# Kernel optimization log

Hardware: AMD Instinct MI355X
Metric: run time of the kernel (lower is better)

## Reference

```python
import jax, jax.numpy as jnp
import numpy as np

K = 3
TAPS = K * K
STD = float(np.sqrt(2.0)) / K  # FilterNorm scale: relu gain / kernel_size


def filter_norm(f, axis):
    # torch FilterNorm: subtract mean, divide by unbiased std (+1e-10), scale by STD
    m = jnp.mean(f, axis=axis, keepdims=True)
    sd = jnp.std(f, axis=axis, keepdims=True, ddof=1)
    return (f - m) / (sd + 1e-10) * STD


def setup_inputs() -> dict:
    key = jax.random.key(0)
    ks = jax.random.split(key, 9)
    B, C, H, W = 4, 64, 192, 192
    mid = int(C * 0.2)  # se_ratio=0.2 -> 12
    f = lambda k, shape, s: jax.random.normal(k, shape, jnp.float32) * s
    return {
        'x':   f(ks[0], (B, C, H, W), 1.0),
        'sw':  f(ks[1], (TAPS, C), 0.05),        # spatial branch 1x1 conv weight
        'sb':  f(ks[2], (TAPS,), 0.05),
        'cw1': f(ks[3], (mid, C), 0.05),         # channel branch squeeze
        'cb1': f(ks[4], (mid,), 0.05),
        'cw2': f(ks[5], (C * TAPS, mid), 0.05),  # channel branch expand
        'cb2': f(ks[6], (C * TAPS,), 0.05),
        'w2':  f(ks[7], (C, C, 1, 9), 0.05),     # trailing 1x9 conv
        'b2':  f(ks[8], (C,), 0.05),
    }


def block_forward(x, sw, sb, cw1, cb1, cw2, cb2, w2, b2):
    B, C, H, W = x.shape
    # --- DDFPack ---
    # spatial filters: 1x1 conv -> (B, 9, H, W), FilterNorm across the 9 taps
    s = jnp.einsum('bchw,tc->bthw', x, sw) + sb[None, :, None, None]
    s = filter_norm(s, axis=1)
    # channel filters: GAP -> 1x1 -> relu -> 1x1 -> (B, C, 9), FilterNorm over taps
    g = x.mean(axis=(2, 3))                         # (B, C)
    h1 = jax.nn.relu(g @ cw1.T + cb1)               # (B, mid)
    cf = (h1 @ cw2.T + cb2).reshape(B, C, TAPS)     # (B, C, 9)
    cf = filter_norm(cf, axis=2)
    # decoupled dynamic filter apply: per-pixel depthwise 3x3, combine='mul', pad=1
    xp = jnp.pad(x, ((0, 0), (0, 0), (1, 1), (1, 1)))
    out = jnp.zeros_like(x)
    for idx in range(TAPS):  # fixed 9-tap loop, no big unfold intermediate
        i, j = idx // K, idx % K
        out = out + xp[:, :, i:i + H, j:j + W] * s[:, idx:idx + 1] * cf[:, :, idx, None, None]
    # --- LeakyReLU(0.1) -> 1x9 conv (pad (0,4)) -> residual add (res_scale=1) ---
    a = jnp.where(out >= 0, out, 0.1 * out)
    y = jax.lax.conv_general_dilated(a, w2, (1, 1), ((0, 0), (4, 4)),
                                     dimension_numbers=('NCHW', 'OIHW', 'NCHW'))
    y = y + b2[None, :, None, None]
    return x + y


def reference(x, sw, sb, cw1, cb1, cw2, cb2, w2, b2):
    return block_forward(x, sw, sb, cw1, cb1, cw2, cb2, w2, b2)
```

## Files before the change

### kernel.cpp

```cpp
#include <hip/hip_runtime.h>
#include <hip/hip_bf16.h>

#define B_    4
#define C_    64
#define H_    192
#define W_    192
#define TAPS_ 9
#define MID_  12
#define HW_   (H_ * W_)
#define K_TOT 576
#define AT_STRIDE 72

constexpr float STD_ = 0.47140452079103173f;

using bf16 = __hip_bfloat16;
typedef __attribute__((ext_vector_type(4))) float  f32x4;
typedef __attribute__((ext_vector_type(8))) short  short8;

__device__ __forceinline__ unsigned short f2bf_bits(float v) {
    union { bf16 h; unsigned short u; } cv;
    cv.h = __float2bfloat16(v);
    return cv.u;
}

__device__ __forceinline__ int at_word(int row, int cw) {
    int key = (row >> 2) & 7;
    return row * (AT_STRIDE / 2) + ((((cw >> 2) ^ key) & 7) << 2) + (cw & 3);
}

__global__ __launch_bounds__(256) void k_pre(const float* __restrict__ x,
                                             const float* __restrict__ w2,
                                             unsigned short* __restrict__ w2bf,
                                             float* __restrict__ partials) {
    int bx = blockIdx.x;
    if (bx < 144) {
        int d = bx * 256 + threadIdx.x;
        int o = d / K_TOT;
        int rem = d - o * K_TOT;
        int t = rem >> 6;
        int c = rem & 63;
        w2bf[d] = f2bf_bits(w2[(o * C_ + c) * TAPS_ + t]);
        return;
    }
    bx -= 144;
    int bc = bx / 3, part = bx - 3 * (bx / 3);
    const float4* p = (const float4*)(x + (size_t)bc * HW_ + part * 12288);
    float s = 0.f;
    #pragma unroll
    for (int k = 0; k < 12; ++k) {
        float4 u = p[threadIdx.x + k * 256];
        s += u.x + u.y + u.z + u.w;
    }
    #pragma unroll
    for (int off = 32; off; off >>= 1) s += __shfl_down(s, off);
    __shared__ float red[4];
    if ((threadIdx.x & 63) == 0) red[threadIdx.x >> 6] = s;
    __syncthreads();
    if (threadIdx.x == 0)
        partials[bx] = red[0] + red[1] + red[2] + red[3];
}

__global__ __launch_bounds__(256) void k_cf(const float* __restrict__ partials,
                                            const float* __restrict__ cw1,
                                            const float* __restrict__ cb1,
                                            const float* __restrict__ cw2,
                                            const float* __restrict__ cb2,
                                            float* __restrict__ cfn) {
    __shared__ float g_l[B_ * C_];
    __shared__ float h1_l[B_ * MID_];
    int tid = threadIdx.x;
    g_l[tid] = (partials[tid * 3] + partials[tid * 3 + 1] + partials[tid * 3 + 2])
               * (1.0f / HW_);
    __syncthreads();
    if (tid < B_ * MID_) {
        int b = tid / MID_, m = tid % MID_;
        float acc = cb1[m];
        for (int c = 0; c < C_; ++c) acc += g_l[b * C_ + c] * cw1[m * C_ + c];
        h1_l[tid] = fmaxf(acc, 0.f);
    }
    __syncthreads();
    int b = tid >> 6, c = tid & 63;
    float f[TAPS_];
    float mean = 0.f;
    #pragma unroll
    for (int t = 0; t < TAPS_; ++t) {
        int n = c * TAPS_ + t;
        float acc = cb2[n];
        #pragma unroll
        for (int m = 0; m < MID_; ++m) acc += h1_l[b * MID_ + m] * cw2[n * MID_ + m];
        f[t] = acc;
        mean += acc;
    }
    mean *= (1.f / TAPS_);
    float var = 0.f;
    #pragma unroll
    for (int t = 0; t < TAPS_; ++t) { float d = f[t] - mean; var += d * d; }
    var *= (1.f / (TAPS_ - 1));
    float scale = STD_ / (sqrtf(fmaxf(var, 0.f)) + 1e-10f);
    #pragma unroll
    for (int t = 0; t < TAPS_; ++t)
        cfn[(b * C_ + c) * TAPS_ + t] = (f[t] - mean) * scale;
}

__global__ __launch_bounds__(256, 3) void k_main(const float* __restrict__ x,
                                                 const float* __restrict__ sw,
                                                 const float* __restrict__ sb,
                                                 const float* __restrict__ cfn,
                                                 const unsigned short* __restrict__ w2bf,
                                                 const float* __restrict__ bias2,
                                                 float* __restrict__ out) {
    __shared__ __align__(16) char smem[36016];
    short*          aT   = (short*)smem;
    unsigned*       aT32 = (unsigned*)smem;
    float*          sw_l = (float*)smem;
    float*          s_l  = (float*)(smem + 28800);
    float*          b2_l = (float*)(smem + 35712);
    float*          sb_l = (float*)(smem + 35968);

    int bh = blockIdx.x;
    int bb = bh / H_;
    int h  = bh - bb * H_;
    int tid = threadIdx.x;
    int lane = tid & 63, wid = tid >> 6;
    int quad = lane >> 4, l16 = lane & 15;
    int obase = wid * 16;

    for (int i = tid; i < TAPS_ * C_; i += 256) sw_l[i] = sw[i];
    if (tid < C_) b2_l[tid] = bias2[tid];
    if (tid < TAPS_) sb_l[tid] = sb[tid];
    __syncthreads();

    const short* w2s = (const short*)w2bf;
    const short* arow = w2s + (obase + l16) * K_TOT + quad * 8;
    short8 a0 = *(const short8*)(arow);
    short8 a1 = *(const short8*)(arow + 32);

    if (tid < W_) {
        int w = tid;
        float acc[TAPS_];
        #pragma unroll
        for (int t = 0; t < TAPS_; ++t) acc[t] = sb_l[t];
        const float* px = x + (size_t)bb * C_ * HW_ + h * W_ + w;
        #pragma unroll 8
        for (int c = 0; c < C_; ++c) {
            float xv = px[(size_t)c * HW_];
            #pragma unroll
            for (int t = 0; t < TAPS_; ++t) acc[t] = fmaf(xv, sw_l[t * C_ + c], acc[t]);
        }
        float mean = 0.f;
        #pragma unroll
        for (int t = 0; t < TAPS_; ++t) mean += acc[t];
        mean *= (1.f / TAPS_);
        float var = 0.f;
        #pragma unroll
        for (int t = 0; t < TAPS_; ++t) { float d = acc[t] - mean; var += d * d; }
        var *= (1.f / (TAPS_ - 1));
        float scale = STD_ / (sqrtf(fmaxf(var, 0.f)) + 1e-10f);
        float* sp = s_l + (w & 3) * 432 + (w >> 2);
        #pragma unroll
        for (int t = 0; t < TAPS_; ++t) sp[t * 48] = (acc[t] - mean) * scale;
    }
    __syncthreads();

    for (int i = tid; i < 8 * (AT_STRIDE / 2); i += 256) {
        int rowIdx = i / (AT_STRIDE / 2);
        int col    = i - rowIdx * (AT_STRIDE / 2);
        int r = (rowIdx < 4) ? rowIdx : (192 + rowIdx);
        aT32[r * (AT_STRIDE / 2) + col] = 0u;
    }

    {
        int wbase = wid * 16;
        if (lane < 48) {
            int w0 = 4 * lane;
            float sreg[4][TAPS_];
            #pragma unroll
            for (int k = 0; k < 4; ++k) {
                const float* sp = s_l + k * 432 + lane;
                #pragma unroll
                for (int t = 0; t < TAPS_; ++t) sreg[k][t] = sp[t * 48];
            }
            bool l0 = (lane == 0), l47 = (lane == 47);
            int rok0 = (h > 0), rok2 = (h < H_ - 1);
            int midx = l0 ? 0 : (w0 - 1);
            int pidx = l47 ? w0 : (w0 + 4);
            const float* xbase = x + (long)bb * C_ * HW_ + (long)(h - 1) * W_;
            #pragma unroll 1
            for (int i = 0; i < 16; i += 2) {
                int c0 = wbase + i;
                int cu = __builtin_amdgcn_readfirstlane(c0);
                const float* cfp = cfn + bb * (C_ * TAPS_) + cu * TAPS_;
                const float* pc0 = xbase + (long)c0 * HW_;
                const float* pc1 = pc0 + HW_;
                float acc0[4] = {0.f, 0.f, 0.f, 0.f};
                float acc1[4] = {0.f, 0.f, 0.f, 0.f};
                #pragma unroll
                for (int r = 0; r < 3; ++r) {
                    if (r == 0 && !rok0) continue;
                    if (r == 2 && !rok2) continue;
                    const float* p0 = pc0 + r * W_;
                    const float* p1 = pc1 + r * W_;
                    float4 fa = *(const float4*)(p0 + w0);
                    float4 fb = *(const float4*)(p1 + w0);
                    float ma = l0 ? 0.f : p0[midx];
                    float mb = l0 ? 0.f : p1[midx];
                    float pa = l47 ? 0.f : p0[pidx];
                    float pb = l47 ? 0.f : p1[pidx];
                    float va[6] = { ma, fa.x, fa.y, fa.z, fa.w, pa };
                    float vb[6] = { mb, fb.x, fb.y, fb.z, fb.w, pb };
                    #pragma unroll
                    for (int dc = 0; dc < 3; ++dc) {
                        int t = r * 3 + dc;
                        float cva = cfp[t];
                        float cvb = cfp[TAPS_ + t];
                        #pragma unroll
                        for (int k = 0; k < 4; ++k) {
                            acc0[k] = fmaf(va[k + dc] * sreg[k][t], cva, acc0[k]);
                            acc1[k] = fmaf(vb[k + dc] * sreg[k][t], cvb, acc1[k]);
                        }
                    }
                }
                int cw = c0 >> 1;
                #pragma unroll
                for (int k = 0; k < 4; ++k) {
                    float a0v = acc0[k]; a0v = (a0v >= 0.f) ? a0v : 0.1f * a0v;
                    float a1v = acc1[k]; a1v = (a1v >= 0.f) ? a1v : 0.1f * a1v;
                    unsigned pk = (unsigned)f2bf_bits(a0v)
                                | ((unsigned)f2bf_bits(a1v) << 16);
                    aT32[at_word(w0 + k + 4, cw)] = pk;
                }
            }
        }
    }
    __syncthreads();

    {
        f32x4 acc[12];
        #pragma unroll
        for (int n = 0; n < 12; ++n) acc[n] = (f32x4){0.f, 0.f, 0.f, 0.f};

        #pragma unroll 1
        for (int kk = 0; kk < 18; ++kk) {
            short8 a2 = a1;
            if (kk < 16) a2 = *(const short8*)(arow + (kk + 2) * 32);
            int t = kk >> 1;
            int ch = ((kk & 1) << 2) + quad;
            int rowb = l16 + t;
            int key0 = (rowb >> 2) & 7;
            int off0 = rowb * AT_STRIDE + (((ch ^ key0) & 7) << 3);
            int off1 = rowb * AT_STRIDE + (((ch ^ key0 ^ 4) & 7) << 3);
            #pragma unroll
            for (int n = 0; n < 12; ++n) {
                int off = ((n & 1) ? off1 : off0) + n * 16 * AT_STRIDE;
                short8 bf = *(const short8*)(aT + off);
                acc[n] = __builtin_amdgcn_mfma_f32_16x16x32_bf16(a0, bf, acc[n], 0, 0, 0);
            }
            a0 = a1; a1 = a2;
        }

        size_t xbase = (size_t)bb * C_ * HW_ + (size_t)h * W_;
        #pragma unroll
        for (int n = 0; n < 12; ++n) {
            int w = n * 16 + l16;
            #pragma unroll
            for (int reg = 0; reg < 4; ++reg) {
                int o = obase + quad * 4 + reg;
                size_t idx = xbase + (size_t)o * HW_ + w;
                out[idx] = acc[n][reg] + b2_l[o] + x[idx];
            }
        }
    }
}

extern "C" void kernel_launch(void* const* d_in, const int* in_sizes, int n_in,
                              void* d_out, int out_size, void* d_ws, size_t ws_size,
                              hipStream_t stream) {
    const float* x   = (const float*)d_in[0];
    const float* sw  = (const float*)d_in[1];
    const float* sb  = (const float*)d_in[2];
    const float* cw1 = (const float*)d_in[3];
    const float* cb1 = (const float*)d_in[4];
    const float* cw2 = (const float*)d_in[5];
    const float* cb2 = (const float*)d_in[6];
    const float* w2  = (const float*)d_in[7];
    const float* b2  = (const float*)d_in[8];
    float* out = (float*)d_out;

    unsigned short* w2bf = (unsigned short*)d_ws;
    float* partials = (float*)((char*)d_ws + 73728);
    float* cfn      = (float*)((char*)d_ws + 76800);

    hipLaunchKernelGGL(k_pre, dim3(912), dim3(256), 0, stream, x, w2, w2bf, partials);
    hipLaunchKernelGGL(k_cf, dim3(1), dim3(256), 0, stream,
                       partials, cw1, cb1, cw2, cb2, cfn);
    hipLaunchKernelGGL(k_main, dim3(B_ * H_), dim3(256), 0, stream,
                       x, sw, sb, cfn, w2bf, b2, out);
}
```

Measured before the change: 145.7 us.

## Repartition 1x9 conv MFMA work so each wave owns all outputs for three width tiles

```diff
diff --git a/kernel.cpp b/kernel.cpp
--- a/kernel.cpp
+++ b/kernel.cpp
@@ -123,17 +123,21 @@
     int tid = threadIdx.x;
     int lane = tid & 63, wid = tid >> 6;
     int quad = lane >> 4, l16 = lane & 15;
-    int obase = wid * 16;
+    int wid3 = wid * 3;
 
     for (int i = tid; i < TAPS_ * C_; i += 256) sw_l[i] = sw[i];
     if (tid < C_) b2_l[tid] = bias2[tid];
     if (tid < TAPS_) sb_l[tid] = sb[tid];
     __syncthreads();
 
-    const short* w2s = (const short*)w2bf;
-    const short* arow = w2s + (obase + l16) * K_TOT + quad * 8;
-    short8 a0 = *(const short8*)(arow);
-    short8 a1 = *(const short8*)(arow + 32);
+    const short* abase = (const short*)w2bf + (size_t)l16 * K_TOT + quad * 8;
+    short8 A0[4], A1[4], A2[4];
+    #pragma unroll
+    for (int of = 0; of < 4; ++of)
+        A0[of] = *(const short8*)(abase + of * 16 * K_TOT + 0 * 32);
+    #pragma unroll
+    for (int of = 0; of < 4; ++of)
+        A1[of] = *(const short8*)(abase + of * 16 * K_TOT + 1 * 32);
 
     if (tid < W_) {
         int w = tid;
@@ -239,34 +243,56 @@
         #pragma unroll
         for (int n = 0; n < 12; ++n) acc[n] = (f32x4){0.f, 0.f, 0.f, 0.f};
 
+#define PHASE_C_BODY(KK, AUSE, ALOAD, KLOAD, DOLOAD)                            \
+        do {                                                                    \
+            if (DOLOAD) {                                                       \
+                ALOAD[0] = *(const short8*)(abase + 0 * 16 * K_TOT + (KLOAD) * 32); \
+                ALOAD[1] = *(const short8*)(abase + 1 * 16 * K_TOT + (KLOAD) * 32); \
+                ALOAD[2] = *(const short8*)(abase + 2 * 16 * K_TOT + (KLOAD) * 32); \
+                ALOAD[3] = *(const short8*)(abase + 3 * 16 * K_TOT + (KLOAD) * 32); \
+            }                                                                   \
+            int t_    = (KK) >> 1;                                              \
+            int ch_   = (((KK) & 1) << 2) + quad;                               \
+            int rowb_ = l16 + t_;                                               \
+            int key0_ = (rowb_ >> 2) & 7;                                       \
+            int off0_ = rowb_ * AT_STRIDE + (((ch_ ^ key0_) & 7) << 3);         \
+            int off1_ = rowb_ * AT_STRIDE + (((ch_ ^ key0_ ^ 4) & 7) << 3);     \
+            _Pragma("unroll")                                                   \
+            for (int nn = 0; nn < 3; ++nn) {                                    \
+                int n_   = wid3 + nn;                                           \
+                int off_ = ((n_ & 1) ? off1_ : off0_) + n_ * 16 * AT_STRIDE;    \
+                short8 bf_ = *(const short8*)(aT + off_);                       \
+                acc[nn * 4 + 0] = __builtin_amdgcn_mfma_f32_16x16x32_bf16(      \
+                    AUSE[0], bf_, acc[nn * 4 + 0], 0, 0, 0);                    \
+                acc[nn * 4 + 1] = __builtin_amdgcn_mfma_f32_16x16x32_bf16(      \
+                    AUSE[1], bf_, acc[nn * 4 + 1], 0, 0, 0);                    \
+                acc[nn * 4 + 2] = __builtin_amdgcn_mfma_f32_16x16x32_bf16(      \
+                    AUSE[2], bf_, acc[nn * 4 + 2], 0, 0, 0);                    \
+                acc[nn * 4 + 3] = __builtin_amdgcn_mfma_f32_16x16x32_bf16(      \
+                    AUSE[3], bf_, acc[nn * 4 + 3], 0, 0, 0);                    \
+            }                                                                   \
+        } while (0)
+
         #pragma unroll 1
-        for (int kk = 0; kk < 18; ++kk) {
-            short8 a2 = a1;
-            if (kk < 16) a2 = *(const short8*)(arow + (kk + 2) * 32);
-            int t = kk >> 1;
-            int ch = ((kk & 1) << 2) + quad;
-            int rowb = l16 + t;
-            int key0 = (rowb >> 2) & 7;
-            int off0 = rowb * AT_STRIDE + (((ch ^ key0) & 7) << 3);
-            int off1 = rowb * AT_STRIDE + (((ch ^ key0 ^ 4) & 7) << 3);
+        for (int kk3 = 0; kk3 < 18; kk3 += 3) {
+            PHASE_C_BODY(kk3 + 0, A0, A2, kk3 + 2, true);
+            PHASE_C_BODY(kk3 + 1, A1, A0, kk3 + 3, (kk3 < 15));
+            PHASE_C_BODY(kk3 + 2, A2, A1, kk3 + 4, (kk3 < 15));
+        }
+#undef PHASE_C_BODY
+
+        size_t xbase = (size_t)bb * C_ * HW_ + (size_t)h * W_;
+        #pragma unroll
+        for (int nn = 0; nn < 3; ++nn) {
+            int w = (wid3 + nn) * 16 + l16;
             #pragma unroll
-            for (int n = 0; n < 12; ++n) {
-                int off = ((n & 1) ? off1 : off0) + n * 16 * AT_STRIDE;
-                short8 bf = *(const short8*)(aT + off);
-                acc[n] = __builtin_amdgcn_mfma_f32_16x16x32_bf16(a0, bf, acc[n], 0, 0, 0);
-            }
-            a0 = a1; a1 = a2;
-        }
-
-        size_t xbase = (size_t)bb * C_ * HW_ + (size_t)h * W_;
-        #pragma unroll
-        for (int n = 0; n < 12; ++n) {
-            int w = n * 16 + l16;
-            #pragma unroll
-            for (int reg = 0; reg < 4; ++reg) {
-                int o = obase + quad * 4 + reg;
-                size_t idx = xbase + (size_t)o * HW_ + w;
-                out[idx] = acc[n][reg] + b2_l[o] + x[idx];
+            for (int of = 0; of < 4; ++of) {
+                #pragma unroll
+                for (int reg = 0; reg < 4; ++reg) {
+                    int o = of * 16 + quad * 4 + reg;
+                    size_t idx = xbase + (size_t)o * HW_ + w;
+                    out[idx] = acc[nn * 4 + of][reg] + b2_l[o] + x[idx];
+                }
             }
         }
     }
```

Result: slower. 175.6 us (+20.5%).

## Split each output row into two width halves per block to raise occupancy

Applied to the files above, without the earlier changes.

```diff
diff --git a/kernel.cpp b/kernel.cpp
--- a/kernel.cpp
+++ b/kernel.cpp
@@ -10,6 +10,8 @@
 #define HW_   (H_ * W_)
 #define K_TOT 576
 #define AT_STRIDE 72
+#define ATROWS 104
+#define WBLK  96
 
 constexpr float STD_ = 0.47140452079103173f;
 
@@ -102,24 +104,30 @@
         cfn[(b * C_ + c) * TAPS_ + t] = (f[t] - mean) * scale;
 }
 
-__global__ __launch_bounds__(256, 3) void k_main(const float* __restrict__ x,
+__global__ __launch_bounds__(256, 6) void k_main(const float* __restrict__ x,
                                                  const float* __restrict__ sw,
                                                  const float* __restrict__ sb,
                                                  const float* __restrict__ cfn,
                                                  const unsigned short* __restrict__ w2bf,
                                                  const float* __restrict__ bias2,
                                                  float* __restrict__ out) {
-    __shared__ __align__(16) char smem[36016];
+    __shared__ __align__(16) char smem[19232];
     short*          aT   = (short*)smem;
     unsigned*       aT32 = (unsigned*)smem;
     float*          sw_l = (float*)smem;
-    float*          s_l  = (float*)(smem + 28800);
-    float*          b2_l = (float*)(smem + 35712);
-    float*          sb_l = (float*)(smem + 35968);
-
-    int bh = blockIdx.x;
+    float*          s_l  = (float*)(smem + 14976);
+    float*          b2_l = (float*)(smem + 18720);
+    float*          sb_l = (float*)(smem + 18976);
+
+    int bx = blockIdx.x;
+    int side = (bx >= B_ * H_) ? 1 : 0;
+    int bh = bx - side * (B_ * H_);
     int bb = bh / H_;
     int h  = bh - bb * H_;
+    int wstart = side * WBLK;
+    int wv0    = side ? (WBLK - 4) : 0;
+    int roff   = side ? 0 : 4;
+
     int tid = threadIdx.x;
     int lane = tid & 63, wid = tid >> 6;
     int quad = lane >> 4, l16 = lane & 15;
@@ -135,8 +143,8 @@
     short8 a0 = *(const short8*)(arow);
     short8 a1 = *(const short8*)(arow + 32);
 
-    if (tid < W_) {
-        int w = tid;
+    if (tid < 100) {
+        int w = wv0 + tid;
         float acc[TAPS_];
         #pragma unroll
         for (int t = 0; t < TAPS_; ++t) acc[t] = sb_l[t];
@@ -156,88 +164,87 @@
         for (int t = 0; t < TAPS_; ++t) { float d = acc[t] - mean; var += d * d; }
         var *= (1.f / (TAPS_ - 1));
         float scale = STD_ / (sqrtf(fmaxf(var, 0.f)) + 1e-10f);
-        float* sp = s_l + (w & 3) * 432 + (w >> 2);
-        #pragma unroll
-        for (int t = 0; t < TAPS_; ++t) sp[t * 48] = (acc[t] - mean) * scale;
-    }
-    __syncthreads();
-
-    for (int i = tid; i < 8 * (AT_STRIDE / 2); i += 256) {
-        int rowIdx = i / (AT_STRIDE / 2);
-        int col    = i - rowIdx * (AT_STRIDE / 2);
-        int r = (rowIdx < 4) ? rowIdx : (192 + rowIdx);
+        float* sp = s_l + (tid & 1) * 468 + (tid >> 1);
+        #pragma unroll
+        for (int t = 0; t < TAPS_; ++t) sp[t * 52] = (acc[t] - mean) * scale;
+    }
+    __syncthreads();
+
+    if (tid < 4 * (AT_STRIDE / 2)) {
+        int rowIdx = tid / (AT_STRIDE / 2);
+        int col    = tid - rowIdx * (AT_STRIDE / 2);
+        int r = (side ? 100 : 0) + rowIdx;
         aT32[r * (AT_STRIDE / 2) + col] = 0u;
     }
 
     {
-        int wbase = wid * 16;
-        if (lane < 48) {
-            int w0 = 4 * lane;
-            float sreg[4][TAPS_];
-            #pragma unroll
-            for (int k = 0; k < 4; ++k) {
-                const float* sp = s_l + k * 432 + lane;
+        int wbase_c = wid * 16;
+        if (lane < 50) {
+            int u0 = 2 * lane;
+            int wp = wv0 + u0;
+            float sreg0[TAPS_], sreg1[TAPS_];
+            {
+                const float* sp0 = s_l + lane;
+                const float* sp1 = s_l + 468 + lane;
                 #pragma unroll
-                for (int t = 0; t < TAPS_; ++t) sreg[k][t] = sp[t * 48];
+                for (int t = 0; t < TAPS_; ++t) { sreg0[t] = sp0[t * 52]; sreg1[t] = sp1[t * 52]; }
             }
-            bool l0 = (lane == 0), l47 = (lane == 47);
+            bool lm = (side == 0) && (lane == 0);
+            bool pm = (side == 1) && (lane == 49);
             int rok0 = (h > 0), rok2 = (h < H_ - 1);
-            int midx = l0 ? 0 : (w0 - 1);
-            int pidx = l47 ? w0 : (w0 + 4);
-            const float* xbase = x + (long)bb * C_ * HW_ + (long)(h - 1) * W_;
+            const float* xbase = x + (long)bb * C_ * HW_ + (long)(h - 1) * W_ + wp;
+            int rb0 = u0 + roff;
             #pragma unroll 1
             for (int i = 0; i < 16; i += 2) {
-                int c0 = wbase + i;
+                int c0 = wbase_c + i;
                 int cu = __builtin_amdgcn_readfirstlane(c0);
                 const float* cfp = cfn + bb * (C_ * TAPS_) + cu * TAPS_;
                 const float* pc0 = xbase + (long)c0 * HW_;
                 const float* pc1 = pc0 + HW_;
-                float acc0[4] = {0.f, 0.f, 0.f, 0.f};
-                float acc1[4] = {0.f, 0.f, 0.f, 0.f};
+                float a00 = 0.f, a01 = 0.f, a10 = 0.f, a11 = 0.f;
                 #pragma unroll
                 for (int r = 0; r < 3; ++r) {
                     if (r == 0 && !rok0) continue;
                     if (r == 2 && !rok2) continue;
                     const float* p0 = pc0 + r * W_;
                     const float* p1 = pc1 + r * W_;
-                    float4 fa = *(const float4*)(p0 + w0);
-                    float4 fb = *(const float4*)(p1 + w0);
-                    float ma = l0 ? 0.f : p0[midx];
-                    float mb = l0 ? 0.f : p1[midx];
-                    float pa = l47 ? 0.f : p0[pidx];
-                    float pb = l47 ? 0.f : p1[pidx];
-                    float va[6] = { ma, fa.x, fa.y, fa.z, fa.w, pa };
-                    float vb[6] = { mb, fb.x, fb.y, fb.z, fb.w, pb };
+                    float2 f0 = *(const float2*)p0;
+                    float2 f1 = *(const float2*)p1;
+                    float m0 = lm ? 0.f : p0[-1];
+                    float m1 = lm ? 0.f : p1[-1];
+                    float q0 = pm ? 0.f : p0[2];
+                    float q1 = pm ? 0.f : p1[2];
+                    float va[4] = { m0, f0.x, f0.y, q0 };
+                    float vb[4] = { m1, f1.x, f1.y, q1 };
                     #pragma unroll
                     for (int dc = 0; dc < 3; ++dc) {
                         int t = r * 3 + dc;
                         float cva = cfp[t];
                         float cvb = cfp[TAPS_ + t];
-                        #pragma unroll
-                        for (int k = 0; k < 4; ++k) {
-                            acc0[k] = fmaf(va[k + dc] * sreg[k][t], cva, acc0[k]);
-                            acc1[k] = fmaf(vb[k + dc] * sreg[k][t], cvb, acc1[k]);
-                        }
+                        a00 = fmaf(va[dc]     * sreg0[t], cva, a00);
+                        a01 = fmaf(va[dc + 1] * sreg1[t], cva, a01);
+                        a10 = fmaf(vb[dc]     * sreg0[t], cvb, a10);
+                        a11 = fmaf(vb[dc + 1] * sreg1[t], cvb, a11);
                     }
                 }
+                a00 = (a00 >= 0.f) ? a00 : 0.1f * a00;
+                a01 = (a01 >= 0.f) ? a01 : 0.1f * a01;
+                a10 = (a10 >= 0.f) ? a10 : 0.1f * a10;
+                a11 = (a11 >= 0.f) ? a11 : 0.1f * a11;
                 int cw = c0 >> 1;
-                #pragma unroll
-                for (int k = 0; k < 4; ++k) {
-                    float a0v = acc0[k]; a0v = (a0v >= 0.f) ? a0v : 0.1f * a0v;
-                    float a1v = acc1[k]; a1v = (a1v >= 0.f) ? a1v : 0.1f * a1v;
-                    unsigned pk = (unsigned)f2bf_bits(a0v)
-                                | ((unsigned)f2bf_bits(a1v) << 16);
-                    aT32[at_word(w0 + k + 4, cw)] = pk;
-                }
+                unsigned pk0 = (unsigned)f2bf_bits(a00) | ((unsigned)f2bf_bits(a10) << 16);
+                unsigned pk1 = (unsigned)f2bf_bits(a01) | ((unsigned)f2bf_bits(a11) << 16);
+                aT32[at_word(rb0,     cw)] = pk0;
+                aT32[at_word(rb0 + 1, cw)] = pk1;
             }
         }
     }
     __syncthreads();
 
     {
-        f32x4 acc[12];
-        #pragma unroll
-        for (int n = 0; n < 12; ++n) acc[n] = (f32x4){0.f, 0.f, 0.f, 0.f};
+        f32x4 acc[6];
+        #pragma unroll
+        for (int n = 0; n < 6; ++n) acc[n] = (f32x4){0.f, 0.f, 0.f, 0.f};
 
         #pragma unroll 1
         for (int kk = 0; kk < 18; ++kk) {
@@ -250,7 +257,7 @@
             int off0 = rowb * AT_STRIDE + (((ch ^ key0) & 7) << 3);
             int off1 = rowb * AT_STRIDE + (((ch ^ key0 ^ 4) & 7) << 3);
             #pragma unroll
-            for (int n = 0; n < 12; ++n) {
+            for (int n = 0; n < 6; ++n) {
                 int off = ((n & 1) ? off1 : off0) + n * 16 * AT_STRIDE;
                 short8 bf = *(const short8*)(aT + off);
                 acc[n] = __builtin_amdgcn_mfma_f32_16x16x32_bf16(a0, bf, acc[n], 0, 0, 0);
@@ -260,8 +267,8 @@
 
         size_t xbase = (size_t)bb * C_ * HW_ + (size_t)h * W_;
         #pragma unroll
-        for (int n = 0; n < 12; ++n) {
-            int w = n * 16 + l16;
+        for (int n = 0; n < 6; ++n) {
+            int w = wstart + n * 16 + l16;
             #pragma unroll
             for (int reg = 0; reg < 4; ++reg) {
                 int o = obase + quad * 4 + reg;
@@ -293,6 +300,6 @@
     hipLaunchKernelGGL(k_pre, dim3(912), dim3(256), 0, stream, x, w2, w2bf, partials);
     hipLaunchKernelGGL(k_cf, dim3(1), dim3(256), 0, stream,
                        partials, cw1, cb1, cw2, cb2, cfn);
-    hipLaunchKernelGGL(k_main, dim3(B_ * H_), dim3(256), 0, stream,
+    hipLaunchKernelGGL(k_main, dim3(B_ * H_ * 2), dim3(256), 0, stream,
                        x, sw, sb, cfn, w2bf, b2, out);
 }
```

After: 160.7 us. 1.1x slower.
